# Performance work log

Hardware: AMD Instinct MI355X
Metric: run time of the kernel (lower is better)

Reference implementation:

```python
import jax, jax.numpy as jnp
import numpy as np

B, E, L = 262144, 16, 224  # pixels, endmembers, spectral bands


def setup_inputs() -> dict:
    key = jax.random.key(0)
    kx, ke, kb = jax.random.split(key, 3)
    x = jax.random.uniform(kx, (B, E), dtype=jnp.float32)          # abundances
    endmembers = jax.random.uniform(ke, (E, L), dtype=jnp.float32)  # spectral signatures
    b_s = jax.random.normal(kb, (B,), dtype=jnp.float32) * 0.1      # per-pixel PPNM coeff
    return {"x": x, "endmembers": endmembers, "b_s": b_s}


def reference(x, endmembers, b_s):
    # mat = x @ W : [B, L]
    mat = jnp.matmul(x, endmembers)
    # Original: mat + transpose(matmul(transpose(mat*mat), diag(b_s)))
    # which is exactly a row-wise scale of mat^2 by b_s.
    return mat + b_s[:, None] * (mat * mat)
```

## Files before the change

kernel.cpp:

```cpp
#include <hip/hip_runtime.h>


#define LBANDS 224
#define EMEMB  16
#define GROUPS 56
#define PROWS  8
#define NTHREADS (GROUPS * PROWS)

__global__ __launch_bounds__(NTHREADS, 4) void ppnm_kernel(
    const float* __restrict__ x,
    const float* __restrict__ w,
    const float* __restrict__ bs,
    float* __restrict__ out,
    int B)
{
    const int t  = threadIdx.x;
    const int g  = t % GROUPS;
    const int pr = t / GROUPS;

    float4 Wf[EMEMB];
    #pragma unroll
    for (int k = 0; k < EMEMB; ++k) {
        Wf[k] = *reinterpret_cast<const float4*>(w + k * LBANDS + 4 * g);
    }

    const int tiles = B / PROWS;
    int tile = blockIdx.x;
    if (tile >= tiles) return;

    int p = tile * PROWS + pr;
    const float4* xr = reinterpret_cast<const float4*>(x + p * EMEMB);
    float4 xa = xr[0], xb = xr[1], xc = xr[2], xd = xr[3];
    float  b  = bs[p];

    for (;;) {
        const int curp = p;
        const float4 ca = xa, cb = xb, cc = xc, cd = xd;
        const float  cbv = b;

        const int next = tile + gridDim.x;
        if (next < tiles) {
            p  = next * PROWS + pr;
            const float4* nr = reinterpret_cast<const float4*>(x + p * EMEMB);
            xa = nr[0]; xb = nr[1]; xc = nr[2]; xd = nr[3];
            b  = bs[p];
        }

        const float xs[EMEMB] = { ca.x, ca.y, ca.z, ca.w,
                                  cb.x, cb.y, cb.z, cb.w,
                                  cc.x, cc.y, cc.z, cc.w,
                                  cd.x, cd.y, cd.z, cd.w };
        float4 acc = make_float4(0.f, 0.f, 0.f, 0.f);
        #pragma unroll
        for (int k = 0; k < EMEMB; ++k) {
            acc.x = fmaf(xs[k], Wf[k].x, acc.x);
            acc.y = fmaf(xs[k], Wf[k].y, acc.y);
            acc.z = fmaf(xs[k], Wf[k].z, acc.z);
            acc.w = fmaf(xs[k], Wf[k].w, acc.w);
        }

        float4 r;
        r.x = fmaf(cbv * acc.x, acc.x, acc.x);
        r.y = fmaf(cbv * acc.y, acc.y, acc.y);
        r.z = fmaf(cbv * acc.z, acc.z, acc.z);
        r.w = fmaf(cbv * acc.w, acc.w, acc.w);

        *reinterpret_cast<float4*>(out + curp * LBANDS + 4 * g) = r;

        if (next >= tiles) break;
        tile = next;
    }
}

extern "C" void kernel_launch(void* const* d_in, const int* in_sizes, int n_in,
                              void* d_out, int out_size, void* d_ws, size_t ws_size,
                              hipStream_t stream) {
    const float* x  = (const float*)d_in[0];
    const float* w  = (const float*)d_in[1];
    const float* bs = (const float*)d_in[2];
    float* out = (float*)d_out;

    const int B = in_sizes[2];

    const int grid = 2048;
    ppnm_kernel<<<grid, NTHREADS, 0, stream>>>(x, w, bs, out, B);
}
```

Measured before the change: 295.8 us.

## Stage per-block x and b_s tiles through double-buffered shared memory

Each block now processes 32 pixels per iteration. A subset of threads loads that tile's x rows and b_s values cooperatively with coalesced float4 reads into a double-buffered LDS array, and all threads then read them back from shared memory. Previously each of the 56 threads in a group loaded the same 64-byte x row directly from global memory, which relied on the caches to absorb the redundant reads. The change adds a __syncthreads per iteration and LDS traffic, and it assumes B is a multiple of 32.

```diff
diff --git a/kernel.cpp b/kernel.cpp
--- a/kernel.cpp
+++ b/kernel.cpp
@@ -4,8 +4,10 @@
 #define LBANDS 224
 #define EMEMB  16
 #define GROUPS 56
-#define PROWS  8
-#define NTHREADS (GROUPS * PROWS)
+#define PPHASE 8
+#define NTHREADS (GROUPS * PPHASE)
+#define PPB    32
+#define XCHUNKS (PPB * 4)
 
 __global__ __launch_bounds__(NTHREADS, 4) void ppnm_kernel(
     const float* __restrict__ x,
@@ -16,7 +18,7 @@
 {
     const int t  = threadIdx.x;
     const int g  = t % GROUPS;
-    const int pr = t / GROUPS;
+    const int pw = t / GROUPS;
 
     float4 Wf[EMEMB];
     #pragma unroll
@@ -24,52 +26,87 @@
         Wf[k] = *reinterpret_cast<const float4*>(w + k * LBANDS + 4 * g);
     }
 
-    const int tiles = B / PROWS;
-    int tile = blockIdx.x;
-    if (tile >= tiles) return;
+    __shared__ float4 xsh[2][XCHUNKS];
+    __shared__ float  bsh[2][PPB];
 
-    int p = tile * PROWS + pr;
-    const float4* xr = reinterpret_cast<const float4*>(x + p * EMEMB);
-    float4 xa = xr[0], xb = xr[1], xc = xr[2], xd = xr[3];
-    float  b  = bs[p];
+    const int bodies  = B / PPB;
+    const int bstride = gridDim.x;
 
+    int body = blockIdx.x;
+    if (body >= bodies) return;
+
+    const float4* xv = reinterpret_cast<const float4*>(x);
+
+    if (t < XCHUNKS) {
+        xsh[0][t] = xv[body * XCHUNKS + t];
+    } else if (t < XCHUNKS + PPB) {
+        bsh[0][t - XCHUNKS] = bs[body * PPB + (t - XCHUNKS)];
+    }
+    __syncthreads();
+
+#define PPNM_FMA4(SCAL, K)                                                    \
+        acc.x = fmaf((SCAL), Wf[K].x, acc.x);                                 \
+        acc.y = fmaf((SCAL), Wf[K].y, acc.y);                                 \
+        acc.z = fmaf((SCAL), Wf[K].z, acc.z);                                 \
+        acc.w = fmaf((SCAL), Wf[K].w, acc.w);
+
+    int cur = 0;
     for (;;) {
-        const int curp = p;
-        const float4 ca = xa, cb = xb, cc = xc, cd = xd;
-        const float  cbv = b;
+        const int nbody     = body + bstride;
+        const bool have_next = (nbody < bodies);
 
-        const int next = tile + gridDim.x;
-        if (next < tiles) {
-            p  = next * PROWS + pr;
-            const float4* nr = reinterpret_cast<const float4*>(x + p * EMEMB);
-            xa = nr[0]; xb = nr[1]; xc = nr[2]; xd = nr[3];
-            b  = bs[p];
+        float4 xstage = make_float4(0.f, 0.f, 0.f, 0.f);
+        float  bstage = 0.f;
+        if (have_next) {
+            if (t < XCHUNKS) {
+                xstage = xv[nbody * XCHUNKS + t];
+            } else if (t < XCHUNKS + PPB) {
+                bstage = bs[nbody * PPB + (t - XCHUNKS)];
+            }
         }
 
-        const float xs[EMEMB] = { ca.x, ca.y, ca.z, ca.w,
-                                  cb.x, cb.y, cb.z, cb.w,
-                                  cc.x, cc.y, cc.z, cc.w,
-                                  cd.x, cd.y, cd.z, cd.w };
-        float4 acc = make_float4(0.f, 0.f, 0.f, 0.f);
         #pragma unroll
-        for (int k = 0; k < EMEMB; ++k) {
-            acc.x = fmaf(xs[k], Wf[k].x, acc.x);
-            acc.y = fmaf(xs[k], Wf[k].y, acc.y);
-            acc.z = fmaf(xs[k], Wf[k].z, acc.z);
-            acc.w = fmaf(xs[k], Wf[k].w, acc.w);
+        for (int j = 0; j < PPB / PPHASE; ++j) {
+            const int px = pw + PPHASE * j;
+            const float4 xa = xsh[cur][px * 4 + 0];
+            const float4 xb = xsh[cur][px * 4 + 1];
+            const float4 xc = xsh[cur][px * 4 + 2];
+            const float4 xd = xsh[cur][px * 4 + 3];
+            const float  sb = bsh[cur][px];
+
+            float4 acc = make_float4(0.f, 0.f, 0.f, 0.f);
+            PPNM_FMA4(xa.x,  0) PPNM_FMA4(xa.y,  1)
+            PPNM_FMA4(xa.z,  2) PPNM_FMA4(xa.w,  3)
+            PPNM_FMA4(xb.x,  4) PPNM_FMA4(xb.y,  5)
+            PPNM_FMA4(xb.z,  6) PPNM_FMA4(xb.w,  7)
+            PPNM_FMA4(xc.x,  8) PPNM_FMA4(xc.y,  9)
+            PPNM_FMA4(xc.z, 10) PPNM_FMA4(xc.w, 11)
+            PPNM_FMA4(xd.x, 12) PPNM_FMA4(xd.y, 13)
+            PPNM_FMA4(xd.z, 14) PPNM_FMA4(xd.w, 15)
+
+            float4 r;
+            r.x = fmaf(sb * acc.x, acc.x, acc.x);
+            r.y = fmaf(sb * acc.y, acc.y, acc.y);
+            r.z = fmaf(sb * acc.z, acc.z, acc.z);
+            r.w = fmaf(sb * acc.w, acc.w, acc.w);
+
+            *reinterpret_cast<float4*>(out + (body * PPB + px) * LBANDS + 4 * g) = r;
         }
 
-        float4 r;
-        r.x = fmaf(cbv * acc.x, acc.x, acc.x);
-        r.y = fmaf(cbv * acc.y, acc.y, acc.y);
-        r.z = fmaf(cbv * acc.z, acc.z, acc.z);
-        r.w = fmaf(cbv * acc.w, acc.w, acc.w);
+        if (!have_next) break;
 
-        *reinterpret_cast<float4*>(out + curp * LBANDS + 4 * g) = r;
+        if (t < XCHUNKS) {
+            xsh[cur ^ 1][t] = xstage;
+        } else if (t < XCHUNKS + PPB) {
+            bsh[cur ^ 1][t - XCHUNKS] = bstage;
+        }
+        __syncthreads();
 
-        if (next >= tiles) break;
-        tile = next;
+        body = nbody;
+        cur ^= 1;
     }
+
+#undef PPNM_FMA4
 }
 
 extern "C" void kernel_launch(void* const* d_in, const int* in_sizes, int n_in,
```

Result: faster. 257.2 us (-13.0%).
